# Kernel tuning notes

Hardware: AMD Instinct MI355X
Metric: run time of the kernel (lower is better)

## Reference

```python
import jax, jax.numpy as jnp
import numpy as np

N = 50000      # nodes
IN = 128       # in_dim
HID = 128      # hidden_dim
HEADS = 4
OUT = HID // HEADS   # per-head out_channels
R = 8          # num_relations
E = 640000     # message-passing edges
E2 = 200000    # decode edge pairs
NC = 8         # num_classes
EPS_LN = 1e-5


def layer_norm(x, g, b):
    m = x.mean(-1, keepdims=True)
    v = ((x - m) ** 2).mean(-1, keepdims=True)
    return (x - m) * jax.lax.rsqrt(v + EPS_LN) * g + b


def rgat_conv(x, edge_index, edge_type, W, q, k, b):
    # PyG RGATConv defaults: additive-self-attention, across-relation softmax,
    # concat=True, negative_slope=0.2, sum aggregation.
    src, dst = edge_index[0], edge_index[1]
    # relation-specific transform for all nodes, then gather per edge
    xw = jnp.einsum('ni,rio->nro', x, W)          # [N, R, HID]
    xi = xw[dst, edge_type]                        # [E, HID] target feats
    xj = xw[src, edge_type]                        # [E, HID] source feats
    alpha = jax.nn.leaky_relu(xi @ q + xj @ k, negative_slope=0.2)  # [E, HEADS]
    # softmax over incoming edges of each destination node (per head)
    amax = jax.ops.segment_max(alpha, dst, num_segments=N)
    amax = jnp.where(jnp.isfinite(amax), amax, 0.0)
    ex = jnp.exp(alpha - amax[dst])
    den = jax.ops.segment_sum(ex, dst, num_segments=N)
    attn = ex / (den[dst] + 1e-16)                 # [E, HEADS]
    msg = (xj.reshape(E, HEADS, OUT) * attn[:, :, None]).reshape(E, HID)
    out = jax.ops.segment_sum(msg, dst, num_segments=N)  # [N, HID]
    return out + b


def setup_inputs() -> dict:
    key = jax.random.key(0)
    ks = jax.random.split(key, 12)
    sI = 1.0 / np.sqrt(IN)
    sH = 1.0 / np.sqrt(HID)
    return {
        'x': jax.random.normal(ks[0], (N, IN), jnp.float32),
        'edge_index': jax.random.randint(ks[1], (2, E), 0, N),
        'edge_type': jax.random.randint(ks[2], (E,), 0, R),
        'edges': jax.random.randint(ks[3], (E2, 2), 0, N),
        'w1': jax.random.normal(ks[4], (R, IN, HID), jnp.float32) * sI,
        'q1': jax.random.normal(ks[5], (HID, HEADS), jnp.float32) * sH,
        'k1': jax.random.normal(ks[6], (HID, HEADS), jnp.float32) * sH,
        'b1': jnp.zeros((HID,), jnp.float32),
        'w2': jax.random.normal(ks[7], (R, HID, HID), jnp.float32) * sH,
        'q2': jax.random.normal(ks[8], (HID, HEADS), jnp.float32) * sH,
        'k2': jax.random.normal(ks[9], (HID, HEADS), jnp.float32) * sH,
        'b2': jnp.zeros((HID,), jnp.float32),
        'ln1_g': jnp.ones((HID,), jnp.float32),
        'ln1_b': jnp.zeros((HID,), jnp.float32),
        'ln2_g': jnp.ones((HID,), jnp.float32),
        'ln2_b': jnp.zeros((HID,), jnp.float32),
        'mw1': jax.random.normal(ks[10], (2 * HID, HID), jnp.float32) / np.sqrt(2 * HID),
        'mb1': jnp.zeros((HID,), jnp.float32),
        'mw2': jax.random.normal(ks[11], (HID, NC), jnp.float32) * sH,
        'mb2': jnp.zeros((NC,), jnp.float32),
    }


def reference(x, edge_index, edge_type, edges,
              w1, q1, k1, b1, w2, q2, k2, b2,
              ln1_g, ln1_b, ln2_g, ln2_b,
              mw1, mb1, mw2, mb2):
    # encode (dropout is identity in eval mode)
    h1 = rgat_conv(x, edge_index, edge_type, w1, q1, k1, b1)
    h1 = layer_norm(jax.nn.relu(h1), ln1_g, ln1_b)
    h2 = rgat_conv(h1, edge_index, edge_type, w2, q2, k2, b2)
    h2 = layer_norm(jax.nn.relu(h2), ln2_g, ln2_b)
    h = h1 + h2
    # decode: gather node pairs, concat, MLP
    z = jnp.concatenate([h[edges[:, 0]], h[edges[:, 1]]], axis=1)  # [E2, 2*HID]
    z = jax.nn.gelu(z @ mw1 + mb1, approximate=False)
    return z @ mw2 + mb2  # [E2, NC]
```

## Files before the change

### kernel.cpp

```cpp
#include <hip/hip_runtime.h>
#include <hip/hip_bf16.h>

#define NN    50000
#define RR    8
#define HIDC  128
#define NHEADS 4
#define EE    640000
#define EE2   200000
#define NCL   8

typedef __hip_bfloat16 bf16;
typedef unsigned short u16;
typedef __attribute__((ext_vector_type(8))) short short8;
typedef __attribute__((ext_vector_type(4))) float floatx4;

__device__ __forceinline__ float us2f(u16 u) {
    return __uint_as_float(((unsigned)u) << 16);
}
__device__ __forceinline__ float bf2f(bf16 v) { return __bfloat162float(v); }
__device__ __forceinline__ u16 f2us(float f) {
    bf16 h = __float2bfloat16(f);
    return *(u16*)&h;
}
__device__ __forceinline__ float ldf(const void* p, int i, bool f32) {
    return f32 ? ((const float*)p)[i] : us2f(((const u16*)p)[i]);
}
__device__ __forceinline__ float wredmax(float v) {
#pragma unroll
    for (int off = 32; off; off >>= 1) v = fmaxf(v, __shfl_xor(v, off));
    return v;
}
__device__ __forceinline__ float wredsum(float v) {
#pragma unroll
    for (int off = 32; off; off >>= 1) v += __shfl_xor(v, off);
    return v;
}

__global__ __launch_bounds__(1024) void k_sniff(const u16* __restrict__ x, int* __restrict__ flags) {
    __shared__ int cnt;
    if (threadIdx.x == 0) cnt = 0;
    __syncthreads();
    int c = 0;
#pragma unroll
    for (int it = 0; it < 8; it++) {
        ushort4 a = ((const ushort4*)x)[(it * 1024 + threadIdx.x) * 2];
        ushort4 b = ((const ushort4*)x)[(it * 1024 + threadIdx.x) * 2 + 1];
        c += (((a.x >> 7) & 0xFF) == 0xFF) + (((a.y >> 7) & 0xFF) == 0xFF)
           + (((a.z >> 7) & 0xFF) == 0xFF) + (((a.w >> 7) & 0xFF) == 0xFF)
           + (((b.x >> 7) & 0xFF) == 0xFF) + (((b.y >> 7) & 0xFF) == 0xFF)
           + (((b.z >> 7) & 0xFF) == 0xFF) + (((b.w >> 7) & 0xFF) == 0xFF);
    }
    c += __shfl_xor(c, 32); c += __shfl_xor(c, 16); c += __shfl_xor(c, 8);
    c += __shfl_xor(c, 4);  c += __shfl_xor(c, 2);  c += __shfl_xor(c, 1);
    if ((threadIdx.x & 63) == 0) atomicAdd(&cnt, c);
    __syncthreads();
    if (threadIdx.x == 0) { flags[0] = (cnt > 16) ? 1 : 0; flags[1] = 1; }
}

__global__ void k_zero(int* __restrict__ p, int n) {
    int i = blockIdx.x * 256 + threadIdx.x;
    if (i < n) p[i] = 0;
}
__global__ void k_hist(const int* __restrict__ ei, int* __restrict__ deg) {
    int e = blockIdx.x * 256 + threadIdx.x;
    if (e < EE) atomicAdd(&deg[ei[EE + e]], 1);
}
__global__ __launch_bounds__(256) void k_scan1(const int* __restrict__ deg,
                                               int* __restrict__ bsum) {
    int i = blockIdx.x * 256 + threadIdx.x;
    int v = (i < NN) ? deg[i] : 0;
    __shared__ int red[4];
    int lane = threadIdx.x & 63, w = threadIdx.x >> 6;
#pragma unroll
    for (int off = 32; off; off >>= 1) v += __shfl_xor(v, off);
    if (lane == 0) red[w] = v;
    __syncthreads();
    if (threadIdx.x == 0) bsum[blockIdx.x] = red[0] + red[1] + red[2] + red[3];
}
__global__ __launch_bounds__(256) void k_scan2(const int* __restrict__ bsum,
                                               int* __restrict__ boff,
                                               int* __restrict__ rowptr) {
    __shared__ int s[256];
    int t = threadIdx.x;
    s[t] = (t < 196) ? bsum[t] : 0;
    __syncthreads();
    for (int off = 1; off < 256; off <<= 1) {
        int u = (t >= off) ? s[t - off] : 0;
        __syncthreads();
        s[t] += u;
        __syncthreads();
    }
    if (t < 196) boff[t] = (t == 0) ? 0 : s[t - 1];
    if (t == 255) rowptr[NN] = s[255];
}
__global__ __launch_bounds__(256) void k_scan3(int* __restrict__ deg ,
                                               const int* __restrict__ boff,
                                               int* __restrict__ rowptr) {
    __shared__ int s[256];
    int t = threadIdx.x;
    int i = blockIdx.x * 256 + t;
    int v = (i < NN) ? deg[i] : 0;
    s[t] = v;
    __syncthreads();
    for (int off = 1; off < 256; off <<= 1) {
        int u = (t >= off) ? s[t - off] : 0;
        __syncthreads();
        s[t] += u;
        __syncthreads();
    }
    if (i < NN) {
        int val = boff[blockIdx.x] + s[t] - v;
        rowptr[i] = val;
        deg[i] = val;
    }
}
__global__ void k_scatter(const int* __restrict__ ei, int* __restrict__ cursor,
                          int* __restrict__ elist) {
    int e = blockIdx.x * 256 + threadIdx.x;
    if (e >= EE) return;
    int pos = atomicAdd(&cursor[ei[EE + e]], 1);
    elist[pos] = e;
}

__global__ void k_qkw(const void* __restrict__ w1, const void* __restrict__ w2,
                      const void* __restrict__ q1, const void* __restrict__ k1,
                      const void* __restrict__ q2, const void* __restrict__ k2,
                      float* __restrict__ qkw, const int* __restrict__ fl) {
    int idx = blockIdx.x * 256 + threadIdx.x;
    if (idx >= 16384) return;
    const bool f = fl[0] != 0;
    int mat = idx >> 10;
    int i   = (idx >> 3) & 127;
    int h8  = idx & 7;
    const void* W = (mat >= 8) ? w2 : w1;
    const void* qk = (mat >= 8) ? ((h8 < 4) ? q2 : k2) : ((h8 < 4) ? q1 : k1);
    int h = h8 & 3;
    int r = mat & 7;
    float acc = 0.f;
    for (int o = 0; o < HIDC; o++)
        acc += ldf(W, (r * HIDC + i) * HIDC + o, f) * ldf(qk, o * NHEADS + h, f);
    qkw[idx] = acc;
}

__global__ void k_wswz(const void* __restrict__ w1, const void* __restrict__ w2,
                       const float* __restrict__ qkw,
                       u16* __restrict__ Wf2, const int* __restrict__ fl) {
    int idx = blockIdx.x * 256 + threadIdx.x;
    if (idx >= 36864) return;
    const bool f = fl[0] != 0;
    int mat = idx / 2304, rest = idx % 2304;
    int c = rest >> 8, q = (rest >> 6) & 3, ln = rest & 63;
    int k0 = q * 32 + (ln >> 4) * 8;
    int nn = c * 16 + (ln & 15);
    int r = mat & 7;
    u16 o[8];
    if (c < 8) {
        const void* W = (mat >= 8) ? w2 : w1;
#pragma unroll
        for (int j = 0; j < 8; j++)
            o[j] = f2us(ldf(W, (r * HIDC + k0 + j) * HIDC + nn, f));
    } else {
        int col = nn - 128;
#pragma unroll
        for (int j = 0; j < 8; j++)
            o[j] = (col < 8) ? f2us(qkw[mat * 1024 + (k0 + j) * 8 + col]) : (u16)0;
    }
    u16* dst = Wf2 + (size_t)mat * 18432 + (size_t)(((c * 4 + q) * 64 + ln) * 8);
    *(ushort4*)dst       = ushort4{o[0], o[1], o[2], o[3]};
    *(ushort4*)(dst + 4) = ushort4{o[4], o[5], o[6], o[7]};
}

__global__ __launch_bounds__(256) void k_xw2(const void* __restrict__ X,
                                             const u16* __restrict__ Wf2,
                                             bf16* __restrict__ xw,
                                             float* __restrict__ sbuf,
                                             float* __restrict__ tbuf,
                                             const int* __restrict__ fx,
                                             int layer) {
    __shared__ u16 Xs[64 * 136];
    __shared__ float Os[64 * 132];
    const int tid = threadIdx.x;
    const int r = blockIdx.y;
    const int n0 = blockIdx.x * 64;
    const bool xf = fx[0] != 0;
    for (int v = tid; v < 2048; v += 256) {
        int row = v >> 5, c4 = (v & 31) * 4, n = n0 + row;
        ushort4 o = {0, 0, 0, 0};
        if (n < NN) {
            if (xf) {
                float4 hv = *(const float4*)((const float*)X + (size_t)n * HIDC + c4);
                o = ushort4{f2us(hv.x), f2us(hv.y), f2us(hv.z), f2us(hv.w)};
            } else {
                o = *(const ushort4*)((const u16*)X + (size_t)n * HIDC + c4);
            }
        }
        *(ushort4*)&Xs[row * 136 + c4] = o;
    }
    __syncthreads();
    const int w = tid >> 6, lane = tid & 63;
    short8 af[4];
#pragma unroll
    for (int q = 0; q < 4; q++)
        af[q] = *(const short8*)&Xs[(16 * w + (lane & 15)) * 136 + q * 32 + (lane >> 4) * 8];
    const u16* Wfr = Wf2 + (size_t)(layer * 8 + r) * 18432;
#pragma unroll
    for (int c = 0; c < 9; c++) {
        floatx4 acc = {0.f, 0.f, 0.f, 0.f};
#pragma unroll
        for (int q = 0; q < 4; q++) {
            short8 bfr = *(const short8*)&Wfr[(size_t)(((c * 4 + q) * 64 + lane) * 8)];
            acc = __builtin_amdgcn_mfma_f32_16x16x32_bf16(af[q], bfr, acc, 0, 0, 0);
        }
        if (c < 8) {
            int col = c * 16 + (lane & 15);
#pragma unroll
            for (int reg = 0; reg < 4; reg++) {
                int p = 16 * w + (lane >> 4) * 4 + reg;
                Os[p * 132 + col] = acc[reg];
            }
        } else {
            int cl = lane & 15;
            if (cl < 8) {
                float* dstp = (cl < 4) ? sbuf : tbuf;
                int h = cl & 3;
#pragma unroll
                for (int reg = 0; reg < 4; reg++) {
                    int p = 16 * w + (lane >> 4) * 4 + reg;
                    int n = n0 + p;
                    if (n < NN) dstp[(size_t)(n * RR + r) * 4 + h] = acc[reg];
                }
            }
        }
    }
    __syncthreads();
    for (int v = tid; v < 2048; v += 256) {
        int row = v >> 5, c4 = (v & 31) * 4, n = n0 + row;
        if (n < NN) {
            float4 hv = *(const float4*)&Os[row * 132 + c4];
            ushort4 o = {f2us(hv.x), f2us(hv.y), f2us(hv.z), f2us(hv.w)};
            *(ushort4*)((u16*)xw + (size_t)(n * RR + r) * HIDC + c4) = o;
        }
    }
}

__global__ __launch_bounds__(256) void k_attn(const int* __restrict__ rowptr,
                                              const int* __restrict__ elist,
                                              const int* __restrict__ ei,
                                              const int* __restrict__ et,
                                              const float* __restrict__ sb,
                                              const float* __restrict__ tb,
                                              const bf16* __restrict__ xw,
                                              const void* __restrict__ b,
                                              const void* __restrict__ g,
                                              const void* __restrict__ bb,
                                              const float* __restrict__ hprev,
                                              float* __restrict__ hout,
                                              const int* __restrict__ fl) {
    const int lane = threadIdx.x & 63;
    const int d = blockIdx.x * 4 + (threadIdx.x >> 6);
    if (d >= NN) return;
    const bool f = fl[0] != 0;
    const int hl = lane >> 4;
    const int start = rowptr[d], end = rowptr[d + 1];
    float m0 = -1e30f, m1 = -1e30f, m2 = -1e30f, m3 = -1e30f;
    float l0 = 0.f, l1 = 0.f, l2 = 0.f, l3 = 0.f;
    float acc0 = 0.f, acc1 = 0.f;
    for (int c0 = start; c0 < end; c0 += 64) {
        int n = end - c0;
        if (n > 64) n = 64;
        float a0, a1, a2, a3;
        int sr = 0;
        if (lane < n) {
            int e = elist[c0 + lane];
            int src = ei[e], r = et[e];
            sr = src * RR + r;
            float4 si = *(const float4*)&sb[(size_t)(d * RR + r) * 4];
            float4 tj = *(const float4*)&tb[(size_t)sr * 4];
            a0 = si.x + tj.x; a0 = a0 >= 0.f ? a0 : 0.2f * a0;
            a1 = si.y + tj.y; a1 = a1 >= 0.f ? a1 : 0.2f * a1;
            a2 = si.z + tj.z; a2 = a2 >= 0.f ? a2 : 0.2f * a2;
            a3 = si.w + tj.w; a3 = a3 >= 0.f ? a3 : 0.2f * a3;
        } else { a0 = a1 = a2 = a3 = -1e30f; }
        float n0 = fmaxf(m0, wredmax(a0));
        float n1 = fmaxf(m1, wredmax(a1));
        float n2 = fmaxf(m2, wredmax(a2));
        float n3 = fmaxf(m3, wredmax(a3));
        float s0 = __expf(m0 - n0), s1 = __expf(m1 - n1);
        float s2 = __expf(m2 - n2), s3 = __expf(m3 - n3);
        float e0 = __expf(a0 - n0), e1 = __expf(a1 - n1);
        float e2 = __expf(a2 - n2), e3 = __expf(a3 - n3);
        l0 = l0 * s0 + wredsum(e0);
        l1 = l1 * s1 + wredsum(e1);
        l2 = l2 * s2 + wredsum(e2);
        l3 = l3 * s3 + wredsum(e3);
        float scl = hl == 0 ? s0 : hl == 1 ? s1 : hl == 2 ? s2 : s3;
        acc0 *= scl; acc1 *= scl;
        for (int j = 0; j < n; j++) {
            int srj = __shfl(sr, j);
            float wx = __shfl(e0, j), wy = __shfl(e1, j);
            float wz = __shfl(e2, j), ww = __shfl(e3, j);
            float wgt = hl == 0 ? wx : hl == 1 ? wy : hl == 2 ? wz : ww;
            ushort2 uv = *(const ushort2*)((const u16*)xw + (size_t)srj * HIDC + lane * 2);
            acc0 += wgt * us2f(uv.x);
            acc1 += wgt * us2f(uv.y);
        }
        m0 = n0; m1 = n1; m2 = n2; m3 = n3;
    }
    float ld = hl == 0 ? l0 : hl == 1 ? l1 : hl == 2 ? l2 : l3;
    float inv = 1.f / (ld + 1e-16f);
    float v0 = acc0 * inv + ldf(b, 2 * lane, f);
    float v1 = acc1 * inv + ldf(b, 2 * lane + 1, f);
    v0 = fmaxf(v0, 0.f);
    v1 = fmaxf(v1, 0.f);
    float mean = wredsum(v0 + v1) * (1.f / 128.f);
    float d0 = v0 - mean, d1 = v1 - mean;
    float rstd = rsqrtf(wredsum(d0 * d0 + d1 * d1) * (1.f / 128.f) + 1e-5f);
    float y0 = d0 * rstd * ldf(g, 2 * lane, f) + ldf(bb, 2 * lane, f);
    float y1 = d1 * rstd * ldf(g, 2 * lane + 1, f) + ldf(bb, 2 * lane + 1, f);
    if (hprev) {
        y0 += hprev[(size_t)d * HIDC + 2 * lane];
        y1 += hprev[(size_t)d * HIDC + 2 * lane + 1];
    }
    *(float2*)&hout[(size_t)d * HIDC + 2 * lane] = float2{y0, y1};
}

__global__ void k_dswz(const void* __restrict__ mw1, const void* __restrict__ mw2,
                       u16* __restrict__ Wf, const int* __restrict__ fl) {
    int idx = blockIdx.x * 256 + threadIdx.x;
    if (idx >= 4352) return;
    const bool f = fl[0] != 0;
    u16 o[8];
    if (idx < 4096) {
        int c = idx >> 9, q = (idx >> 6) & 7, ln = idx & 63;
        int k0 = q * 32 + (ln >> 4) * 8;
        int nn = c * 16 + (ln & 15);
#pragma unroll
        for (int j = 0; j < 8; j++)
            o[j] = f2us(ldf(mw1, (k0 + j) * HIDC + nn, f));
    } else {
        int fidx = idx - 4096;
        int q = fidx >> 6, ln = fidx & 63;
        int k0 = q * 32 + (ln >> 4) * 8;
        int nn = ln & 15;
#pragma unroll
        for (int j = 0; j < 8; j++)
            o[j] = (nn < 8) ? f2us(ldf(mw2, (k0 + j) * NCL + nn, f)) : (u16)0;
    }
    *(ushort4*)&Wf[idx * 8]     = ushort4{o[0], o[1], o[2], o[3]};
    *(ushort4*)&Wf[idx * 8 + 4] = ushort4{o[4], o[5], o[6], o[7]};
}

__global__ __launch_bounds__(256) void k_decode2(const float* __restrict__ h,
                                                 const int* __restrict__ edges,
                                                 const u16* __restrict__ Wf,
                                                 const void* __restrict__ mb1,
                                                 const void* __restrict__ mb2,
                                                 void* __restrict__ out,
                                                 const int* __restrict__ fl) {
    __shared__ u16 zsu[64 * 136];
    const int tid = threadIdx.x;
    const bool f = fl[0] != 0;
    const int p0 = blockIdx.x * 64;
    const int w = tid >> 6, lane = tid & 63;
    const int m = 16 * w + (lane & 15);
    const int g = lane >> 4;
    const int na = edges[(size_t)(p0 + m) * 2];
    const int nb = edges[(size_t)(p0 + m) * 2 + 1];
    short8 af[8];
#pragma unroll
    for (int q = 0; q < 8; q++) {
        int k0 = q * 32 + g * 8;
        const float* src = h + (size_t)((k0 >> 7) ? nb : na) * HIDC + (k0 & 127);
        float4 a = *(const float4*)src;
        float4 bq = *(const float4*)(src + 4);
        u16 tmp[8] = {f2us(a.x), f2us(a.y), f2us(a.z), f2us(a.w),
                      f2us(bq.x), f2us(bq.y), f2us(bq.z), f2us(bq.w)};
        af[q] = *(short8*)tmp;
    }
#pragma unroll
    for (int c = 0; c < 8; c++) {
        floatx4 acc = {0.f, 0.f, 0.f, 0.f};
#pragma unroll
        for (int q = 0; q < 8; q++) {
            short8 bfr = *(const short8*)&Wf[(size_t)(((c * 8 + q) * 64 + lane) * 8)];
            acc = __builtin_amdgcn_mfma_f32_16x16x32_bf16(af[q], bfr, acc, 0, 0, 0);
        }
        int col = c * 16 + (lane & 15);
        float bv = ldf(mb1, col, f);
#pragma unroll
        for (int reg = 0; reg < 4; reg++) {
            int p = 16 * w + (lane >> 4) * 4 + reg;
            float z = acc[reg] + bv;
            zsu[p * 136 + col] = f2us(0.5f * z * (1.f + erff(z * 0.70710678118654752f)));
        }
    }
    floatx4 acc2 = {0.f, 0.f, 0.f, 0.f};
#pragma unroll
    for (int q = 0; q < 4; q++) {
        short8 af2 = *(const short8*)&zsu[m * 136 + q * 32 + g * 8];
        short8 bfr2 = *(const short8*)&Wf[32768 + (size_t)((q * 64 + lane) * 8)];
        acc2 = __builtin_amdgcn_mfma_f32_16x16x32_bf16(af2, bfr2, acc2, 0, 0, 0);
    }
    int col16 = lane & 15;
    if (col16 < 8) {
        float bv2 = ldf(mb2, col16, f);
#pragma unroll
        for (int reg = 0; reg < 4; reg++) {
            int p = 16 * w + (lane >> 4) * 4 + reg;
            float sv = acc2[reg] + bv2;
            size_t oi = (size_t)(p0 + p) * NCL + col16;
            if (f) ((float*)out)[oi] = sv;
            else   ((bf16*)out)[oi] = __float2bfloat16(sv);
        }
    }
}

extern "C" void kernel_launch(void* const* d_in, const int* in_sizes, int n_in,
                              void* d_out, int out_size, void* d_ws, size_t ws_size,
                              hipStream_t stream) {
    (void)in_sizes; (void)n_in; (void)out_size; (void)ws_size;
    const void* x    = d_in[0];
    const int* ei    = (const int*)d_in[1];
    const int* et    = (const int*)d_in[2];
    const int* edges = (const int*)d_in[3];
    const void* w1 = d_in[4];
    const void* q1 = d_in[5];
    const void* k1 = d_in[6];
    const void* b1 = d_in[7];
    const void* w2 = d_in[8];
    const void* q2 = d_in[9];
    const void* k2 = d_in[10];
    const void* b2 = d_in[11];
    const void* ln1g = d_in[12];
    const void* ln1b = d_in[13];
    const void* ln2g = d_in[14];
    const void* ln2b = d_in[15];
    const void* mw1 = d_in[16];
    const void* mb1 = d_in[17];
    const void* mw2 = d_in[18];
    const void* mb2 = d_in[19];

    char* ws = (char*)d_ws;
    bf16* xwb   = (bf16*)ws;
    u16* Wf     = (u16*)ws;
    float* sbuf = (float*)(ws + 102400000);
    float* tbuf = (float*)(ws + 108800000);
    float* h1   = (float*)(ws + 115200000);
    float* hsum = (float*)(ws + 140800000);
    u16* Wf2    = (u16*)(ws + 140800000);
    int* rowptr = (int*)(ws + 166400000);
    int* cursor = (int*)(ws + 166600016);
    int* elist  = (int*)(ws + 166800016);
    float* qkw  = (float*)(ws + 169360016);
    int* bsum   = (int*)qkw;
    int* boff   = bsum + 256;
    int* flags  = (int*)(ws + 169425552);

    k_sniff<<<1, 1024, 0, stream>>>((const u16*)x, flags);

    k_zero<<<196, 256, 0, stream>>>(cursor, NN);
    k_hist<<<2500, 256, 0, stream>>>(ei, cursor);
    k_scan1<<<196, 256, 0, stream>>>(cursor, bsum);
    k_scan2<<<1, 256, 0, stream>>>(bsum, boff, rowptr);
    k_scan3<<<196, 256, 0, stream>>>(cursor, boff, rowptr);
    k_scatter<<<2500, 256, 0, stream>>>(ei, cursor, elist);
    k_qkw<<<64, 256, 0, stream>>>(w1, w2, q1, k1, q2, k2, qkw, flags);
    k_wswz<<<144, 256, 0, stream>>>(w1, w2, qkw, Wf2, flags);

    for (int layer = 0; layer < 2; ++layer) {
        const void* b  = layer ? b2 : b1;
        const void* lg = layer ? ln2g : ln1g;
        const void* lb = layer ? ln2b : ln1b;
        k_xw2<<<dim3(782, 8), 256, 0, stream>>>(layer ? (const void*)h1 : x, Wf2, xwb,
                                                sbuf, tbuf,
                                                layer ? flags + 1 : flags, layer);
        k_attn<<<12500, 256, 0, stream>>>(rowptr, elist, ei, et, sbuf, tbuf, xwb,
                                          b, lg, lb,
                                          layer ? h1 : (const float*)nullptr,
                                          layer ? hsum : h1, flags);
    }
    k_dswz<<<17, 256, 0, stream>>>(mw1, mw2, Wf, flags);
    k_decode2<<<3125, 256, 0, stream>>>(hsum, edges, Wf, mb1, mb2, d_out, flags);
}
```

Measured before the change: 558.8 us.

## Process four edges concurrently per wavefront in attention aggregation

New measurement: 596.0 us. +6.7%, slower.

```diff
diff --git a/kernel.cpp b/kernel.cpp
--- a/kernel.cpp
+++ b/kernel.cpp
@@ -256,15 +256,21 @@
                                               const float* __restrict__ hprev,
                                               float* __restrict__ hout,
                                               const int* __restrict__ fl) {
-    const int lane = threadIdx.x & 63;
-    const int d = blockIdx.x * 4 + (threadIdx.x >> 6);
+    __shared__ float ews[4][64 * 4];
+    __shared__ int srs[4][64];
+    const int tid = threadIdx.x;
+    const int lane = tid & 63;
+    const int w = tid >> 6;
+    const int d = blockIdx.x * 4 + w;
     if (d >= NN) return;
     const bool f = fl[0] != 0;
-    const int hl = lane >> 4;
+    const int l = lane & 15;
+    const int gg = lane >> 4;
+    const int hh = l >> 2;
     const int start = rowptr[d], end = rowptr[d + 1];
     float m0 = -1e30f, m1 = -1e30f, m2 = -1e30f, m3 = -1e30f;
     float l0 = 0.f, l1 = 0.f, l2 = 0.f, l3 = 0.f;
-    float acc0 = 0.f, acc1 = 0.f;
+    float acc[8] = {};
     for (int c0 = start; c0 < end; c0 += 64) {
         int n = end - c0;
         if (n > 64) n = 64;
@@ -293,35 +299,61 @@
         l1 = l1 * s1 + wredsum(e1);
         l2 = l2 * s2 + wredsum(e2);
         l3 = l3 * s3 + wredsum(e3);
-        float scl = hl == 0 ? s0 : hl == 1 ? s1 : hl == 2 ? s2 : s3;
-        acc0 *= scl; acc1 *= scl;
-        for (int j = 0; j < n; j++) {
-            int srj = __shfl(sr, j);
-            float wx = __shfl(e0, j), wy = __shfl(e1, j);
-            float wz = __shfl(e2, j), ww = __shfl(e3, j);
-            float wgt = hl == 0 ? wx : hl == 1 ? wy : hl == 2 ? wz : ww;
-            ushort2 uv = *(const ushort2*)((const u16*)xw + (size_t)srj * HIDC + lane * 2);
-            acc0 += wgt * us2f(uv.x);
-            acc1 += wgt * us2f(uv.y);
+        *(float4*)&ews[w][lane * 4] = float4{e0, e1, e2, e3};
+        srs[w][lane] = sr;
+        float scl = hh == 0 ? s0 : hh == 1 ? s1 : hh == 2 ? s2 : s3;
+#pragma unroll
+        for (int i = 0; i < 8; i++) acc[i] *= scl;
+        for (int el = gg; el < n; el += 4) {
+            float wv = ews[w][el * 4 + hh];
+            int row = srs[w][el];
+            const u16* p = (const u16*)xw + (size_t)row * HIDC + l * 8;
+            ushort4 ua = *(const ushort4*)p;
+            ushort4 ub = *(const ushort4*)(p + 4);
+            acc[0] += wv * us2f(ua.x); acc[1] += wv * us2f(ua.y);
+            acc[2] += wv * us2f(ua.z); acc[3] += wv * us2f(ua.w);
+            acc[4] += wv * us2f(ub.x); acc[5] += wv * us2f(ub.y);
+            acc[6] += wv * us2f(ub.z); acc[7] += wv * us2f(ub.w);
         }
         m0 = n0; m1 = n1; m2 = n2; m3 = n3;
     }
-    float ld = hl == 0 ? l0 : hl == 1 ? l1 : hl == 2 ? l2 : l3;
+#pragma unroll
+    for (int i = 0; i < 8; i++) {
+        acc[i] += __shfl_xor(acc[i], 16);
+        acc[i] += __shfl_xor(acc[i], 32);
+    }
+    float ld = hh == 0 ? l0 : hh == 1 ? l1 : hh == 2 ? l2 : l3;
     float inv = 1.f / (ld + 1e-16f);
-    float v0 = acc0 * inv + ldf(b, 2 * lane, f);
-    float v1 = acc1 * inv + ldf(b, 2 * lane + 1, f);
-    v0 = fmaxf(v0, 0.f);
-    v1 = fmaxf(v1, 0.f);
-    float mean = wredsum(v0 + v1) * (1.f / 128.f);
-    float d0 = v0 - mean, d1 = v1 - mean;
-    float rstd = rsqrtf(wredsum(d0 * d0 + d1 * d1) * (1.f / 128.f) + 1e-5f);
-    float y0 = d0 * rstd * ldf(g, 2 * lane, f) + ldf(bb, 2 * lane, f);
-    float y1 = d1 * rstd * ldf(g, 2 * lane + 1, f) + ldf(bb, 2 * lane + 1, f);
-    if (hprev) {
-        y0 += hprev[(size_t)d * HIDC + 2 * lane];
-        y1 += hprev[(size_t)d * HIDC + 2 * lane + 1];
-    }
-    *(float2*)&hout[(size_t)d * HIDC + 2 * lane] = float2{y0, y1};
+    float v[8];
+#pragma unroll
+    for (int i = 0; i < 8; i++)
+        v[i] = fmaxf(acc[i] * inv + ldf(b, l * 8 + i, f), 0.f);
+    float sum = 0.f;
+#pragma unroll
+    for (int i = 0; i < 8; i++) sum += v[i];
+#pragma unroll
+    for (int off = 8; off; off >>= 1) sum += __shfl_xor(sum, off);
+    float mean = sum * (1.f / 128.f);
+    float sq = 0.f;
+#pragma unroll
+    for (int i = 0; i < 8; i++) { v[i] -= mean; sq += v[i] * v[i]; }
+#pragma unroll
+    for (int off = 8; off; off >>= 1) sq += __shfl_xor(sq, off);
+    float rstd = rsqrtf(sq * (1.f / 128.f) + 1e-5f);
+    if (gg == 0) {
+        float y[8];
+#pragma unroll
+        for (int i = 0; i < 8; i++)
+            y[i] = v[i] * rstd * ldf(g, l * 8 + i, f) + ldf(bb, l * 8 + i, f);
+        if (hprev) {
+            float4 ha = *(const float4*)&hprev[(size_t)d * HIDC + l * 8];
+            float4 hb = *(const float4*)&hprev[(size_t)d * HIDC + l * 8 + 4];
+            y[0] += ha.x; y[1] += ha.y; y[2] += ha.z; y[3] += ha.w;
+            y[4] += hb.x; y[5] += hb.y; y[6] += hb.z; y[7] += hb.w;
+        }
+        *(float4*)&hout[(size_t)d * HIDC + l * 8]     = float4{y[0], y[1], y[2], y[3]};
+        *(float4*)&hout[(size_t)d * HIDC + l * 8 + 4] = float4{y[4], y[5], y[6], y[7]};
+    }
 }
 
 __global__ void k_dswz(const void* __restrict__ mw1, const void* __restrict__ mw2,
```
